# Kernel tuning notes

Measured on AMD Instinct MI355X. Metric: run time of the kernel, lower is better.

## Reference

```python
import jax, jax.numpy as jnp
import numpy as np

E = 8        # num_experts (== num_local_experts here)
H = 2048     # hidden_size
I = 1024     # intermediate_size
T = 8192     # num_tokens
K = 2        # top_k


def setup_inputs() -> dict:
    key = jax.random.key(0)
    ks = jax.random.split(key, 6)
    x = jax.random.normal(ks[0], (T, H), dtype=jnp.float32)
    selected_experts = jax.random.randint(ks[1], (T, K), 0, E, dtype=jnp.int32)
    routing_weights = jax.random.uniform(ks[2], (T, K), dtype=jnp.float32)
    # per-expert weights; torch Linear stores [out, in]; we store [E, in, out] for einsum
    gate_w = jax.random.normal(ks[3], (E, H, I), dtype=jnp.float32) * 0.02
    up_w = jax.random.normal(ks[4], (E, H, I), dtype=jnp.float32) * 0.02
    down_w = jax.random.normal(ks[5], (E, I, H), dtype=jnp.float32) * 0.02
    return {
        "x": x,
        "selected_experts": selected_experts,
        "routing_weights": routing_weights,
        "gate_w": gate_w,
        "up_w": up_w,
        "down_w": down_w,
    }


def reference(x, selected_experts, routing_weights, gate_w, up_w, down_w):
    # Combined per-(token, expert) weight: sum of routing weights over top-k slots
    # that selected this expert. Mathematically identical to the sort/dispatch/
    # weighted index_add_ in the original module.
    w = jnp.einsum(
        "tke,tk->te",
        jax.nn.one_hot(selected_experts, E, dtype=x.dtype),
        routing_weights.astype(x.dtype),
    )  # [T, E]
    g = jnp.einsum("th,ehi->eti", x, gate_w)               # [E, T, I]
    u = jnp.einsum("th,ehi->eti", x, up_w)                 # [E, T, I]
    a = jax.nn.gelu(g, approximate=True) * u               # gelu tanh approx
    # down-proj per expert then weighted combine (scatter-add equivalent)
    out = jnp.einsum("eti,eih,te->th", a, down_w, w)       # [T, H], float32
    return out
```

## Files before the change

kernel.cpp:

```cpp
#include <hip/hip_runtime.h>
#include <hip/hip_bf16.h>


typedef __attribute__((ext_vector_type(8))) short bf16x8;
typedef __attribute__((ext_vector_type(4))) float f32x4;

#define AS1 __attribute__((address_space(1)))
#define AS3 __attribute__((address_space(3)))

static constexpr int T_TOK = 8192;
static constexpr int HID   = 2048;
static constexpr int INTER = 1024;
static constexpr int NEXP  = 8;
static constexpr int NPAIR = T_TOK * 2;
static constexpr int TM    = 256;
static constexpr int MAX_ROWS = NPAIR + NEXP * TM;
static constexpr int MAX_RT   = MAX_ROWS / TM;
static constexpr int OUTN = T_TOK * HID;

__device__ __forceinline__ unsigned short f2bf(float f) {
  unsigned u = __float_as_uint(f);
  u += 0x7fffu + ((u >> 16) & 1u);
  return (unsigned short)(u >> 16);
}
__device__ __forceinline__ float bf2f(unsigned short h) {
  return __uint_as_float(((unsigned)h) << 16);
}
__device__ __forceinline__ void glds16(const void* g, void* l) {
  __builtin_amdgcn_global_load_lds((const AS1 void*)g, (AS3 void*)l, 16, 0, 0);
}

__global__ void detect_k(const unsigned* __restrict__ xw, int* __restrict__ flagp) {
  int tid = threadIdx.x;
  int cnt = 0;
  for (int i = tid; i < 256; i += 64) {
    unsigned e = (xw[i] >> 7) & 0xffu;
    cnt += (e >= 0x70u && e <= 0x8fu) ? 1 : 0;
  }
  for (int off = 32; off; off >>= 1) cnt += __shfl_down(cnt, off);
  if (tid == 0) *flagp = (cnt >= 192) ? 1 : 0;
}

__global__ void zero_out_k(unsigned* __restrict__ out, const int* __restrict__ flagp) {
  int n = (*flagp) ? (OUTN / 2) : OUTN;
  int i = blockIdx.x * 256 + threadIdx.x;
  int stride = gridDim.x * 256;
  for (; i < n; i += stride) out[i] = 0u;
}

__global__ void routing_k(const int* __restrict__ sel, const void* __restrict__ rwv,
                          int* __restrict__ rows, float* __restrict__ wgt,
                          int* __restrict__ offs, const int* __restrict__ flagp) {
  __shared__ int cnt[NEXP], cur[NEXP], offs_s[NEXP + 1];
  int flag = *flagp;
  const unsigned short* rw16 = (const unsigned short*)rwv;
  const float* rwf = (const float*)rwv;
  int tid = threadIdx.x;
  if (tid < NEXP) cnt[tid] = 0;
  __syncthreads();
  for (int p = tid; p < NPAIR; p += 256) atomicAdd(&cnt[sel[p]], 1);
  __syncthreads();
  if (tid == 0) {
    int off = 0;
    for (int e = 0; e < NEXP; ++e) {
      offs_s[e] = off; cur[e] = off;
      off += (cnt[e] + TM - 1) / TM * TM;
    }
    offs_s[NEXP] = off;
  }
  __syncthreads();
  if (tid <= NEXP) offs[tid] = offs_s[tid];
  for (int p = tid; p < NPAIR; p += 256) {
    int e = sel[p];
    int pos = atomicAdd(&cur[e], 1);
    rows[pos] = p >> 1;
    wgt[pos] = flag ? bf2f(rw16[p]) : rwf[p];
  }
  for (int e = 0; e < NEXP; ++e)
    for (int r = offs_s[e] + cnt[e] + tid; r < offs_s[e + 1]; r += 256) {
      rows[r] = 0; wgt[r] = 0.f;
    }
}

__global__ void convert_x_k(const void* __restrict__ xin,
                            unsigned short* __restrict__ xc,
                            const int* __restrict__ flagp) {
  int flag = *flagp;
  const int nvec = (T_TOK * HID) / 8;
  int v = blockIdx.x * 256 + threadIdx.x;
  int stride = gridDim.x * 256;
  for (; v < nvec; v += stride) {
    if (flag) {
      ((uint4*)xc)[v] = ((const uint4*)xin)[v];
    } else {
      const float4* s = (const float4*)xin;
      float4 a = s[2 * v], b = s[2 * v + 1];
      uint4 o;
      o.x = (unsigned)f2bf(a.x) | ((unsigned)f2bf(a.y) << 16);
      o.y = (unsigned)f2bf(a.z) | ((unsigned)f2bf(a.w) << 16);
      o.z = (unsigned)f2bf(b.x) | ((unsigned)f2bf(b.y) << 16);
      o.w = (unsigned)f2bf(b.z) | ((unsigned)f2bf(b.w) << 16);
      ((uint4*)xc)[v] = o;
    }
  }
}

__global__ void transpose_k(const void* __restrict__ in,
                            unsigned short* __restrict__ out, int R, int C,
                            const int* __restrict__ flagp) {
  __shared__ unsigned short tile[64][65];
  int flag = *flagp;
  int e = blockIdx.z;
  int c0 = blockIdx.x * 64, r0 = blockIdx.y * 64;
  int tid = threadIdx.x;
  if (flag) {
    const unsigned short* src = (const unsigned short*)in + (size_t)e * R * C;
    int tx = tid & 7, ty = tid >> 3;
#pragma unroll
    for (int i = 0; i < 2; ++i) {
      int rr = ty + i * 32;
      uint4 v = *(const uint4*)(src + (size_t)(r0 + rr) * C + c0 + tx * 8);
      unsigned short* t = &tile[rr][tx * 8];
      t[0] = (unsigned short)v.x; t[1] = (unsigned short)(v.x >> 16);
      t[2] = (unsigned short)v.y; t[3] = (unsigned short)(v.y >> 16);
      t[4] = (unsigned short)v.z; t[5] = (unsigned short)(v.z >> 16);
      t[6] = (unsigned short)v.w; t[7] = (unsigned short)(v.w >> 16);
    }
  } else {
    const float* src = (const float*)in + (size_t)e * R * C;
    int tx = tid & 15, ty = tid >> 4;
#pragma unroll
    for (int i = 0; i < 4; ++i) {
      int rr = ty + i * 16;
      float4 v = *(const float4*)(src + (size_t)(r0 + rr) * C + c0 + tx * 4);
      unsigned short* t = &tile[rr][tx * 4];
      t[0] = f2bf(v.x); t[1] = f2bf(v.y); t[2] = f2bf(v.z); t[3] = f2bf(v.w);
    }
  }
  __syncthreads();
  unsigned short* dst = out + (size_t)e * R * C;
  int tx = tid & 7, ty = tid >> 3;
#pragma unroll
  for (int i = 0; i < 2; ++i) {
    int cc = ty + i * 32;
    unsigned short a0 = tile[tx * 8 + 0][cc], a1 = tile[tx * 8 + 1][cc];
    unsigned short a2 = tile[tx * 8 + 2][cc], a3 = tile[tx * 8 + 3][cc];
    unsigned short a4 = tile[tx * 8 + 4][cc], a5 = tile[tx * 8 + 5][cc];
    unsigned short a6 = tile[tx * 8 + 6][cc], a7 = tile[tx * 8 + 7][cc];
    uint4 v;
    v.x = a0 | ((unsigned)a1 << 16); v.y = a2 | ((unsigned)a3 << 16);
    v.z = a4 | ((unsigned)a5 << 16); v.w = a6 | ((unsigned)a7 << 16);
    *(uint4*)(dst + (size_t)(c0 + cc) * R + r0 + tx * 8) = v;
  }
}


__device__ __forceinline__ const bf16x8* ldf(const unsigned short* sm, int slot,
                                             int r, int c8) {
  return (const bf16x8*)(sm + slot * 8192 + r * 64 + ((c8 ^ (r & 7)) << 3));
}
__device__ __forceinline__ void stage_half(const unsigned short* p0,
                                           const unsigned short* p1,
                                           unsigned short* dst) {
  glds16(p0, dst);
  glds16(p1, dst + 4096);
}

#define MFMA8(AH, BH, B)                                                       \
  _Pragma("unroll") for (int i_ = 0; i_ < 4; ++i_) {                           \
    _Pragma("unroll") for (int j_ = 0; j_ < 2; ++j_) {                         \
      acc[AH][BH][i_][j_] = __builtin_amdgcn_mfma_f32_16x16x32_bf16(           \
          a[i_][0], B[j_][0], acc[AH][BH][i_][j_], 0, 0, 0);                   \
      acc[AH][BH][i_][j_] = __builtin_amdgcn_mfma_f32_16x16x32_bf16(           \
          a[i_][1], B[j_][1], acc[AH][BH][i_][j_], 0, 0, 0);                   \
    }                                                                          \
  }

template <int BUF, bool S1, bool S2, int VM>
__device__ __forceinline__ void ktile(
    unsigned short* sm, int wbase, int rA, int rB, int lquad,
    const unsigned short* pA00, const unsigned short* pA01,
    const unsigned short* pA10, const unsigned short* pA11,
    const unsigned short* pB00, const unsigned short* pB01,
    const unsigned short* pB10, const unsigned short* pB11,
    int ko1, int ko2, f32x4 (&acc)[2][2][4][2]) {
  bf16x8 a[4][2], b0[2][2], b1[2][2];
#pragma unroll
  for (int i = 0; i < 4; ++i)
#pragma unroll
    for (int k = 0; k < 2; ++k)
      a[i][k] = *ldf(sm, BUF * 2 + 0, rA + i * 16, k * 4 + lquad);
#pragma unroll
  for (int j = 0; j < 2; ++j)
#pragma unroll
    for (int k = 0; k < 2; ++k)
      b0[j][k] = *ldf(sm, 4 + BUF * 2 + 0, rB + j * 16, k * 4 + lquad);
  if constexpr (S1)
    stage_half(pA10 + ko1, pA11 + ko1, sm + ((BUF ^ 1) * 2 + 1) * 8192 + wbase);
  __builtin_amdgcn_s_barrier();
  asm volatile("s_waitcnt lgkmcnt(0)" ::: "memory");
  __builtin_amdgcn_s_setprio(1);
  MFMA8(0, 0, b0);
  __builtin_amdgcn_s_setprio(0);
  __builtin_amdgcn_s_barrier();
#pragma unroll
  for (int j = 0; j < 2; ++j)
#pragma unroll
    for (int k = 0; k < 2; ++k)
      b1[j][k] = *ldf(sm, 4 + BUF * 2 + 1, rB + j * 16, k * 4 + lquad);
  if constexpr (S1)
    stage_half(pB00 + ko1, pB01 + ko1, sm + (4 + (BUF ^ 1) * 2 + 0) * 8192 + wbase);
  __builtin_amdgcn_s_barrier();
  asm volatile("s_waitcnt lgkmcnt(0)" ::: "memory");
  __builtin_amdgcn_s_setprio(1);
  MFMA8(0, 1, b1);
  __builtin_amdgcn_s_setprio(0);
  __builtin_amdgcn_s_barrier();
#pragma unroll
  for (int i = 0; i < 4; ++i)
#pragma unroll
    for (int k = 0; k < 2; ++k)
      a[i][k] = *ldf(sm, BUF * 2 + 1, rA + i * 16, k * 4 + lquad);
  if constexpr (S2)
    stage_half(pA00 + ko2, pA01 + ko2, sm + (BUF * 2 + 0) * 8192 + wbase);
  __builtin_amdgcn_s_barrier();
  asm volatile("s_waitcnt lgkmcnt(0)" ::: "memory");
  __builtin_amdgcn_s_setprio(1);
  MFMA8(1, 1, b1);
  __builtin_amdgcn_s_setprio(0);
  __builtin_amdgcn_s_barrier();
  if constexpr (S2)
    stage_half(pB10 + ko2, pB11 + ko2, sm + (4 + BUF * 2 + 1) * 8192 + wbase);
  __builtin_amdgcn_s_barrier();
  __builtin_amdgcn_s_setprio(1);
  MFMA8(1, 0, b0);
  __builtin_amdgcn_s_setprio(0);
  if constexpr (VM == 4)
    asm volatile("s_waitcnt vmcnt(4)" ::: "memory");
  else if constexpr (VM == 0)
    asm volatile("s_waitcnt vmcnt(0)" ::: "memory");
  __builtin_amdgcn_s_barrier();
}

__global__ __launch_bounds__(512, 2) void gemm_gateup8(
    const unsigned short* __restrict__ xc,
    const unsigned short* __restrict__ gwT,
    const unsigned short* __restrict__ uwT,
    const int* __restrict__ rows, const int* __restrict__ offs,
    unsigned short* __restrict__ act) {
  extern __shared__ unsigned short sm[];
  int nRT = offs[NEXP] >> 8;
  int rowTile = blockIdx.x >> 3;
  if (rowTile >= nRT) return;
  int nt = blockIdx.x & 7;
  int row0 = rowTile << 8;
  int e = 0;
  while (row0 >= offs[e + 1]) ++e;

  int tid = threadIdx.x;
  int lane = tid & 63, lrow = lane & 15, lquad = lane >> 4;
  int wave = tid >> 6;
  int wmg = wave >> 2, wng = wave & 3;
  int wbase = wave << 9;
  int rA = wmg * 64 + lrow;
  int rB = wng * 32 + lrow;

  int sr = tid >> 3;
  int swz = ((tid & 7) ^ (sr & 7)) << 3;

  const unsigned short* pA00 = xc + (size_t)rows[row0 + sr] * HID + swz;
  const unsigned short* pA01 = xc + (size_t)rows[row0 + 64 + sr] * HID + swz;
  const unsigned short* pA10 = xc + (size_t)rows[row0 + 128 + sr] * HID + swz;
  const unsigned short* pA11 = xc + (size_t)rows[row0 + 192 + sr] * HID + swz;
  const unsigned short* gB = gwT + ((size_t)e * INTER + (size_t)nt * 128) * HID;
  const unsigned short* uB = uwT + ((size_t)e * INTER + (size_t)nt * 128) * HID;
  const unsigned short* pB00 = gB + (size_t)sr * HID + swz;
  const unsigned short* pB01 = gB + (size_t)(64 + sr) * HID + swz;
  const unsigned short* pB10 = uB + (size_t)sr * HID + swz;
  const unsigned short* pB11 = uB + (size_t)(64 + sr) * HID + swz;

  f32x4 acc[2][2][4][2] = {};

  stage_half(pA00, pA01, sm + 0 * 8192 + wbase);
  stage_half(pB00, pB01, sm + 4 * 8192 + wbase);
  stage_half(pB10, pB11, sm + 5 * 8192 + wbase);
  stage_half(pA10, pA11, sm + 1 * 8192 + wbase);
  stage_half(pA00 + 64, pA01 + 64, sm + 2 * 8192 + wbase);
  stage_half(pB10 + 64, pB11 + 64, sm + 7 * 8192 + wbase);
  asm volatile("s_waitcnt vmcnt(4)" ::: "memory");
  __builtin_amdgcn_s_barrier();

  constexpr int NT = HID / 64;
#pragma unroll 1
  for (int it = 0; it < NT / 2 - 1; ++it) {
    int u = it * 2;
    ktile<0, true, true, 4>(sm, wbase, rA, rB, lquad, pA00, pA01, pA10, pA11,
                            pB00, pB01, pB10, pB11, (u + 1) * 64, (u + 2) * 64, acc);
    ktile<1, true, true, 4>(sm, wbase, rA, rB, lquad, pA00, pA01, pA10, pA11,
                            pB00, pB01, pB10, pB11, (u + 2) * 64, (u + 3) * 64, acc);
  }
  ktile<0, true, false, 0>(sm, wbase, rA, rB, lquad, pA00, pA01, pA10, pA11,
                           pB00, pB01, pB10, pB11, (NT - 1) * 64, 0, acc);
  ktile<1, false, false, -1>(sm, wbase, rA, rB, lquad, pA00, pA01, pA10, pA11,
                             pB00, pB01, pB10, pB11, 0, 0, acc);

  size_t actb = (size_t)row0 * INTER + (size_t)nt * 128 + wng * 32 + lrow;
#pragma unroll
  for (int ah = 0; ah < 2; ++ah)
#pragma unroll
    for (int i = 0; i < 4; ++i)
#pragma unroll
      for (int r = 0; r < 4; ++r) {
        int m = ah * 128 + wmg * 64 + i * 16 + lquad * 4 + r;
#pragma unroll
        for (int j = 0; j < 2; ++j) {
          float g = acc[ah][0][i][j][r], u = acc[ah][1][i][j][r];
          float z = 1.5957691f * (g + 0.044715f * g * g * g);
          float aout = g * u / (1.f + __expf(-z));
          act[actb + (size_t)m * INTER + j * 16] = f2bf(aout);
        }
      }
}

__global__ __launch_bounds__(512, 2) void gemm_down8(
    const unsigned short* __restrict__ act,
    const unsigned short* __restrict__ dwT,
    const int* __restrict__ rows, const float* __restrict__ wgt,
    const int* __restrict__ offs, void* __restrict__ outv,
    const int* __restrict__ flagp) {
  extern __shared__ unsigned short sm[];
  int nRT = offs[NEXP] >> 8;
  int rowTile = blockIdx.x >> 3;
  if (rowTile >= nRT) return;
  int nt = blockIdx.x & 7;
  int row0 = rowTile << 8;
  int e = 0;
  while (row0 >= offs[e + 1]) ++e;

  int tid = threadIdx.x;
  int lane = tid & 63, lrow = lane & 15, lquad = lane >> 4;
  int wave = tid >> 6;
  int wmg = wave >> 2, wng = wave & 3;
  int wbase = wave << 9;
  int rA = wmg * 64 + lrow;
  int rB = wng * 32 + lrow;

  int sr = tid >> 3;
  int swz = ((tid & 7) ^ (sr & 7)) << 3;

  const unsigned short* pA00 = act + (size_t)(row0 + sr) * INTER + swz;
  const unsigned short* pA01 = act + (size_t)(row0 + 64 + sr) * INTER + swz;
  const unsigned short* pA10 = act + (size_t)(row0 + 128 + sr) * INTER + swz;
  const unsigned short* pA11 = act + (size_t)(row0 + 192 + sr) * INTER + swz;
  const unsigned short* dB = dwT + ((size_t)e * HID + (size_t)nt * 256) * INTER;
  const unsigned short* pB00 = dB + (size_t)sr * INTER + swz;
  const unsigned short* pB01 = dB + (size_t)(64 + sr) * INTER + swz;
  const unsigned short* pB10 = dB + (size_t)(128 + sr) * INTER + swz;
  const unsigned short* pB11 = dB + (size_t)(192 + sr) * INTER + swz;

  f32x4 acc[2][2][4][2] = {};

  stage_half(pA00, pA01, sm + 0 * 8192 + wbase);
  stage_half(pB00, pB01, sm + 4 * 8192 + wbase);
  stage_half(pB10, pB11, sm + 5 * 8192 + wbase);
  stage_half(pA10, pA11, sm + 1 * 8192 + wbase);
  stage_half(pA00 + 64, pA01 + 64, sm + 2 * 8192 + wbase);
  stage_half(pB10 + 64, pB11 + 64, sm + 7 * 8192 + wbase);
  asm volatile("s_waitcnt vmcnt(4)" ::: "memory");
  __builtin_amdgcn_s_barrier();

  constexpr int NT = INTER / 64;
#pragma unroll 1
  for (int it = 0; it < NT / 2 - 1; ++it) {
    int u = it * 2;
    ktile<0, true, true, 4>(sm, wbase, rA, rB, lquad, pA00, pA01, pA10, pA11,
                            pB00, pB01, pB10, pB11, (u + 1) * 64, (u + 2) * 64, acc);
    ktile<1, true, true, 4>(sm, wbase, rA, rB, lquad, pA00, pA01, pA10, pA11,
                            pB00, pB01, pB10, pB11, (u + 2) * 64, (u + 3) * 64, acc);
  }
  ktile<0, true, false, 0>(sm, wbase, rA, rB, lquad, pA00, pA01, pA10, pA11,
                           pB00, pB01, pB10, pB11, (NT - 1) * 64, 0, acc);
  ktile<1, false, false, -1>(sm, wbase, rA, rB, lquad, pA00, pA01, pA10, pA11,
                             pB00, pB01, pB10, pB11, 0, 0, acc);

  int flag = *flagp;
#pragma unroll
  for (int ah = 0; ah < 2; ++ah)
#pragma unroll
    for (int i = 0; i < 4; ++i)
#pragma unroll
      for (int r = 0; r < 4; ++r) {
        int m = row0 + ah * 128 + wmg * 64 + i * 16 + lquad * 4 + r;
        float w = wgt[m];
        int token = rows[m];
        size_t base = (size_t)token * HID + (size_t)nt * 256 + wng * 32 + lrow;
        if (flag) {
#pragma unroll
          for (int bh = 0; bh < 2; ++bh)
#pragma unroll
            for (int j = 0; j < 2; ++j) {
              float v = acc[ah][bh][i][j][r] * w;
              float o = __shfl_xor(v, 1);
              if (((lane & 1) == 0) && w != 0.f) {
                unsigned* p = (unsigned*)((unsigned short*)outv + base + bh * 128 + j * 16);
                unsigned old = __atomic_load_n(p, __ATOMIC_RELAXED), assumed;
                do {
                  assumed = old;
                  float flo = bf2f((unsigned short)(assumed & 0xffffu));
                  float fhi = bf2f((unsigned short)(assumed >> 16));
                  unsigned nw = (unsigned)f2bf(flo + v) | ((unsigned)f2bf(fhi + o) << 16);
                  old = atomicCAS(p, assumed, nw);
                } while (old != assumed);
              }
            }
        } else {
          if (w != 0.f) {
            float* outf = (float*)outv;
#pragma unroll
            for (int bh = 0; bh < 2; ++bh)
#pragma unroll
              for (int j = 0; j < 2; ++j)
                atomicAdd(outf + base + bh * 128 + j * 16, acc[ah][bh][i][j][r] * w);
          }
        }
      }
}

extern "C" void kernel_launch(void* const* d_in, const int* in_sizes, int n_in,
                              void* d_out, int out_size, void* d_ws, size_t ws_size,
                              hipStream_t stream) {
  (void)in_sizes; (void)n_in; (void)out_size; (void)ws_size;
  const void* x   = d_in[0];
  const int* sel  = (const int*)d_in[1];
  const void* rw  = d_in[2];
  const void* gw  = d_in[3];
  const void* uw  = d_in[4];
  const void* dw  = d_in[5];

  char* ws = (char*)d_ws;
  int* offs  = (int*)ws;
  int* flagp = (int*)(ws + 64);
  int* rows  = (int*)(ws + 256);
  float* wgt = (float*)(ws + 256 + MAX_ROWS * 4);
  unsigned short* gwT = (unsigned short*)(ws + 256 + MAX_ROWS * 8);
  unsigned short* uwT = gwT + (size_t)NEXP * HID * INTER;
  unsigned short* dwT = uwT + (size_t)NEXP * HID * INTER;
  unsigned short* xc  = dwT + (size_t)NEXP * HID * INTER;
  unsigned short* act = xc + (size_t)T_TOK * HID;

  hipFuncSetAttribute(reinterpret_cast<const void*>(gemm_gateup8),
                      hipFuncAttributeMaxDynamicSharedMemorySize, 131072);
  hipFuncSetAttribute(reinterpret_cast<const void*>(gemm_down8),
                      hipFuncAttributeMaxDynamicSharedMemorySize, 131072);

  detect_k<<<1, 64, 0, stream>>>((const unsigned*)x, flagp);
  zero_out_k<<<4096, 256, 0, stream>>>((unsigned*)d_out, flagp);
  routing_k<<<1, 256, 0, stream>>>(sel, rw, rows, wgt, offs, flagp);
  transpose_k<<<dim3(INTER / 64, HID / 64, NEXP), 256, 0, stream>>>(gw, gwT, HID, INTER, flagp);
  transpose_k<<<dim3(INTER / 64, HID / 64, NEXP), 256, 0, stream>>>(uw, uwT, HID, INTER, flagp);
  transpose_k<<<dim3(HID / 64, INTER / 64, NEXP), 256, 0, stream>>>(dw, dwT, INTER, HID, flagp);
  convert_x_k<<<4096, 256, 0, stream>>>(x, xc, flagp);
  gemm_gateup8<<<MAX_RT * 8, 512, 131072, stream>>>(xc, gwT, uwT, rows, offs, act);
  gemm_down8<<<MAX_RT * 8, 512, 131072, stream>>>(act, dwT, rows, wgt, offs, d_out, flagp);
}
```

Before: 691.5 us.

## Replace atomic scatter-add in down GEMM with per-row buffer and combine kernel

```diff
diff --git a/kernel.cpp b/kernel.cpp
--- a/kernel.cpp
+++ b/kernel.cpp
@@ -4,6 +4,7 @@
 
 typedef __attribute__((ext_vector_type(8))) short bf16x8;
 typedef __attribute__((ext_vector_type(4))) float f32x4;
+typedef __attribute__((ext_vector_type(4))) unsigned short us4;
 
 #define AS1 __attribute__((address_space(1)))
 #define AS3 __attribute__((address_space(3)))
@@ -50,7 +51,8 @@
 
 __global__ void routing_k(const int* __restrict__ sel, const void* __restrict__ rwv,
                           int* __restrict__ rows, float* __restrict__ wgt,
-                          int* __restrict__ offs, const int* __restrict__ flagp) {
+                          int* __restrict__ offs, int* __restrict__ pairpos,
+                          const int* __restrict__ flagp) {
   __shared__ int cnt[NEXP], cur[NEXP], offs_s[NEXP + 1];
   int flag = *flagp;
   const unsigned short* rw16 = (const unsigned short*)rwv;
@@ -58,7 +60,7 @@
   int tid = threadIdx.x;
   if (tid < NEXP) cnt[tid] = 0;
   __syncthreads();
-  for (int p = tid; p < NPAIR; p += 256) atomicAdd(&cnt[sel[p]], 1);
+  for (int p = tid; p < NPAIR; p += 1024) atomicAdd(&cnt[sel[p]], 1);
   __syncthreads();
   if (tid == 0) {
     int off = 0;
@@ -70,14 +72,15 @@
   }
   __syncthreads();
   if (tid <= NEXP) offs[tid] = offs_s[tid];
-  for (int p = tid; p < NPAIR; p += 256) {
+  for (int p = tid; p < NPAIR; p += 1024) {
     int e = sel[p];
     int pos = atomicAdd(&cur[e], 1);
     rows[pos] = p >> 1;
     wgt[pos] = flag ? bf2f(rw16[p]) : rwf[p];
+    pairpos[p] = pos;
   }
   for (int e = 0; e < NEXP; ++e)
-    for (int r = offs_s[e] + cnt[e] + tid; r < offs_s[e + 1]; r += 256) {
+    for (int r = offs_s[e] + cnt[e] + tid; r < offs_s[e + 1]; r += 1024) {
       rows[r] = 0; wgt[r] = 0.f;
     }
 }
@@ -108,50 +111,42 @@
 __global__ void transpose_k(const void* __restrict__ in,
                             unsigned short* __restrict__ out, int R, int C,
                             const int* __restrict__ flagp) {
-  __shared__ unsigned short tile[64][65];
+  __shared__ unsigned short t[64 * 72];
   int flag = *flagp;
   int e = blockIdx.z;
   int c0 = blockIdx.x * 64, r0 = blockIdx.y * 64;
   int tid = threadIdx.x;
+  int mr = tid >> 4;
+  int mc = tid & 15;
+  unsigned short b[4][4];
   if (flag) {
     const unsigned short* src = (const unsigned short*)in + (size_t)e * R * C;
-    int tx = tid & 7, ty = tid >> 3;
-#pragma unroll
-    for (int i = 0; i < 2; ++i) {
-      int rr = ty + i * 32;
-      uint4 v = *(const uint4*)(src + (size_t)(r0 + rr) * C + c0 + tx * 8);
-      unsigned short* t = &tile[rr][tx * 8];
-      t[0] = (unsigned short)v.x; t[1] = (unsigned short)(v.x >> 16);
-      t[2] = (unsigned short)v.y; t[3] = (unsigned short)(v.y >> 16);
-      t[4] = (unsigned short)v.z; t[5] = (unsigned short)(v.z >> 16);
-      t[6] = (unsigned short)v.w; t[7] = (unsigned short)(v.w >> 16);
+#pragma unroll
+    for (int i = 0; i < 4; ++i) {
+      us4 v = *(const us4*)(src + (size_t)(r0 + mr * 4 + i) * C + c0 + mc * 4);
+      b[i][0] = v[0]; b[i][1] = v[1]; b[i][2] = v[2]; b[i][3] = v[3];
     }
   } else {
     const float* src = (const float*)in + (size_t)e * R * C;
-    int tx = tid & 15, ty = tid >> 4;
 #pragma unroll
     for (int i = 0; i < 4; ++i) {
-      int rr = ty + i * 16;
-      float4 v = *(const float4*)(src + (size_t)(r0 + rr) * C + c0 + tx * 4);
-      unsigned short* t = &tile[rr][tx * 4];
-      t[0] = f2bf(v.x); t[1] = f2bf(v.y); t[2] = f2bf(v.z); t[3] = f2bf(v.w);
+      float4 v = *(const float4*)(src + (size_t)(r0 + mr * 4 + i) * C + c0 + mc * 4);
+      b[i][0] = f2bf(v.x); b[i][1] = f2bf(v.y); b[i][2] = f2bf(v.z); b[i][3] = f2bf(v.w);
     }
   }
+#pragma unroll
+  for (int j = 0; j < 4; ++j) {
+    us4 w;
+    w[0] = b[0][j]; w[1] = b[1][j]; w[2] = b[2][j]; w[3] = b[3][j];
+    *(us4*)(&t[(mc * 4 + j) * 72 + mr * 4]) = w;
+  }
   __syncthreads();
-  unsigned short* dst = out + (size_t)e * R * C;
-  int tx = tid & 7, ty = tid >> 3;
-#pragma unroll
-  for (int i = 0; i < 2; ++i) {
-    int cc = ty + i * 32;
-    unsigned short a0 = tile[tx * 8 + 0][cc], a1 = tile[tx * 8 + 1][cc];
-    unsigned short a2 = tile[tx * 8 + 2][cc], a3 = tile[tx * 8 + 3][cc];
-    unsigned short a4 = tile[tx * 8 + 4][cc], a5 = tile[tx * 8 + 5][cc];
-    unsigned short a6 = tile[tx * 8 + 6][cc], a7 = tile[tx * 8 + 7][cc];
-    uint4 v;
-    v.x = a0 | ((unsigned)a1 << 16); v.y = a2 | ((unsigned)a3 << 16);
-    v.z = a4 | ((unsigned)a5 << 16); v.w = a6 | ((unsigned)a7 << 16);
-    *(uint4*)(dst + (size_t)(c0 + cc) * R + r0 + tx * 8) = v;
-  }
+  int orow = tid >> 2, ch = (tid & 3) * 16;
+  uint4 v0 = *(const uint4*)(&t[orow * 72 + ch]);
+  uint4 v1 = *(const uint4*)(&t[orow * 72 + ch + 8]);
+  unsigned short* dst = out + (size_t)e * R * C + (size_t)(c0 + orow) * R + r0 + ch;
+  *(uint4*)(dst) = v0;
+  *(uint4*)(dst + 8) = v1;
 }
 
 
@@ -322,12 +317,13 @@
       }
 }
 
+template <int EPI>
 __global__ __launch_bounds__(512, 2) void gemm_down8(
     const unsigned short* __restrict__ act,
     const unsigned short* __restrict__ dwT,
     const int* __restrict__ rows, const float* __restrict__ wgt,
     const int* __restrict__ offs, void* __restrict__ outv,
-    const int* __restrict__ flagp) {
+    const int* __restrict__ flagp, float* __restrict__ y) {
   extern __shared__ unsigned short sm[];
   int nRT = offs[NEXP] >> 8;
   int rowTile = blockIdx.x >> 3;
@@ -383,53 +379,97 @@
   ktile<1, false, false, -1>(sm, wbase, rA, rB, lquad, pA00, pA01, pA10, pA11,
                              pB00, pB01, pB10, pB11, 0, 0, acc);
 
-  int flag = *flagp;
-#pragma unroll
-  for (int ah = 0; ah < 2; ++ah)
-#pragma unroll
-    for (int i = 0; i < 4; ++i)
-#pragma unroll
-      for (int r = 0; r < 4; ++r) {
-        int m = row0 + ah * 128 + wmg * 64 + i * 16 + lquad * 4 + r;
-        float w = wgt[m];
-        int token = rows[m];
-        size_t base = (size_t)token * HID + (size_t)nt * 256 + wng * 32 + lrow;
-        if (flag) {
+  if constexpr (EPI == 1) {
+#pragma unroll
+    for (int ah = 0; ah < 2; ++ah)
+#pragma unroll
+      for (int i = 0; i < 4; ++i)
+#pragma unroll
+        for (int r = 0; r < 4; ++r) {
+          int m = row0 + ah * 128 + wmg * 64 + i * 16 + lquad * 4 + r;
+          float w = wgt[m];
+          float* yp = y + (size_t)m * HID + (size_t)nt * 256 + wng * 32 + lrow;
 #pragma unroll
           for (int bh = 0; bh < 2; ++bh)
 #pragma unroll
-            for (int j = 0; j < 2; ++j) {
-              float v = acc[ah][bh][i][j][r] * w;
-              float o = __shfl_xor(v, 1);
-              if (((lane & 1) == 0) && w != 0.f) {
-                unsigned* p = (unsigned*)((unsigned short*)outv + base + bh * 128 + j * 16);
-                unsigned old = __atomic_load_n(p, __ATOMIC_RELAXED), assumed;
-                do {
-                  assumed = old;
-                  float flo = bf2f((unsigned short)(assumed & 0xffffu));
-                  float fhi = bf2f((unsigned short)(assumed >> 16));
-                  unsigned nw = (unsigned)f2bf(flo + v) | ((unsigned)f2bf(fhi + o) << 16);
-                  old = atomicCAS(p, assumed, nw);
-                } while (old != assumed);
+            for (int j = 0; j < 2; ++j)
+              yp[bh * 128 + j * 16] = acc[ah][bh][i][j][r] * w;
+        }
+  } else {
+    int flag = *flagp;
+#pragma unroll
+    for (int ah = 0; ah < 2; ++ah)
+#pragma unroll
+      for (int i = 0; i < 4; ++i)
+#pragma unroll
+        for (int r = 0; r < 4; ++r) {
+          int m = row0 + ah * 128 + wmg * 64 + i * 16 + lquad * 4 + r;
+          float w = wgt[m];
+          int token = rows[m];
+          size_t base = (size_t)token * HID + (size_t)nt * 256 + wng * 32 + lrow;
+          if (flag) {
+#pragma unroll
+            for (int bh = 0; bh < 2; ++bh)
+#pragma unroll
+              for (int j = 0; j < 2; ++j) {
+                float v = acc[ah][bh][i][j][r] * w;
+                float o = __shfl_xor(v, 1);
+                if (((lane & 1) == 0) && w != 0.f) {
+                  unsigned* p = (unsigned*)((unsigned short*)outv + base + bh * 128 + j * 16);
+                  unsigned old = __atomic_load_n(p, __ATOMIC_RELAXED), assumed;
+                  do {
+                    assumed = old;
+                    float flo = bf2f((unsigned short)(assumed & 0xffffu));
+                    float fhi = bf2f((unsigned short)(assumed >> 16));
+                    unsigned nw = (unsigned)f2bf(flo + v) | ((unsigned)f2bf(fhi + o) << 16);
+                    old = atomicCAS(p, assumed, nw);
+                  } while (old != assumed);
+                }
               }
+          } else {
+            if (w != 0.f) {
+              float* outf = (float*)outv;
+#pragma unroll
+              for (int bh = 0; bh < 2; ++bh)
+#pragma unroll
+                for (int j = 0; j < 2; ++j)
+                  atomicAdd(outf + base + bh * 128 + j * 16, acc[ah][bh][i][j][r] * w);
             }
-        } else {
-          if (w != 0.f) {
-            float* outf = (float*)outv;
-#pragma unroll
-            for (int bh = 0; bh < 2; ++bh)
-#pragma unroll
-              for (int j = 0; j < 2; ++j)
-                atomicAdd(outf + base + bh * 128 + j * 16, acc[ah][bh][i][j][r] * w);
           }
         }
-      }
+  }
+}
+
+__global__ void combine_k(const float* __restrict__ y,
+                          const int* __restrict__ pairpos,
+                          void* __restrict__ outv, const int* __restrict__ flagp) {
+  int flag = *flagp;
+  const int NV = T_TOK * (HID / 4);
+  int v = blockIdx.x * 256 + threadIdx.x;
+  int stride = gridDim.x * 256;
+  for (; v < NV; v += stride) {
+    int t = v >> 9;
+    int hq = (v & 511) * 4;
+    int p0 = pairpos[2 * t], p1 = pairpos[2 * t + 1];
+    float4 a = *(const float4*)(y + (size_t)p0 * HID + hq);
+    float4 b = *(const float4*)(y + (size_t)p1 * HID + hq);
+    float4 s;
+    s.x = a.x + b.x; s.y = a.y + b.y; s.z = a.z + b.z; s.w = a.w + b.w;
+    if (flag) {
+      uint2 o;
+      o.x = (unsigned)f2bf(s.x) | ((unsigned)f2bf(s.y) << 16);
+      o.y = (unsigned)f2bf(s.z) | ((unsigned)f2bf(s.w) << 16);
+      *(uint2*)((unsigned short*)outv + (size_t)v * 4) = o;
+    } else {
+      *(float4*)((float*)outv + (size_t)v * 4) = s;
+    }
+  }
 }
 
 extern "C" void kernel_launch(void* const* d_in, const int* in_sizes, int n_in,
                               void* d_out, int out_size, void* d_ws, size_t ws_size,
                               hipStream_t stream) {
-  (void)in_sizes; (void)n_in; (void)out_size; (void)ws_size;
+  (void)in_sizes; (void)n_in; (void)out_size;
   const void* x   = d_in[0];
   const int* sel  = (const int*)d_in[1];
   const void* rw  = d_in[2];
@@ -438,28 +478,44 @@
   const void* dw  = d_in[5];
 
   char* ws = (char*)d_ws;
-  int* offs  = (int*)ws;
-  int* flagp = (int*)(ws + 64);
-  int* rows  = (int*)(ws + 256);
-  float* wgt = (float*)(ws + 256 + MAX_ROWS * 4);
-  unsigned short* gwT = (unsigned short*)(ws + 256 + MAX_ROWS * 8);
+  int* offs     = (int*)ws;
+  int* flagp    = (int*)(ws + 64);
+  int* rows     = (int*)(ws + 256);
+  float* wgt    = (float*)(ws + 256 + MAX_ROWS * 4);
+  int* pairpos  = (int*)(ws + 256 + MAX_ROWS * 8);
+  size_t off0   = 256 + (size_t)MAX_ROWS * 8 + (size_t)NPAIR * 4;
+  off0 = (off0 + 255) & ~(size_t)255;
+  unsigned short* dwT = (unsigned short*)(ws + off0);
+  unsigned short* act = dwT + (size_t)NEXP * HID * INTER;
+  unsigned short* gwT = act + (size_t)MAX_ROWS * INTER;
   unsigned short* uwT = gwT + (size_t)NEXP * HID * INTER;
-  unsigned short* dwT = uwT + (size_t)NEXP * HID * INTER;
-  unsigned short* xc  = dwT + (size_t)NEXP * HID * INTER;
-  unsigned short* act = xc + (size_t)T_TOK * HID;
+  unsigned short* xc  = uwT + (size_t)NEXP * HID * INTER;
+  float* y            = (float*)gwT;
+  size_t y_end = ((char*)gwT - ws) + (size_t)MAX_ROWS * HID * 4;
+  bool use_y = ws_size >= y_end;
 
   hipFuncSetAttribute(reinterpret_cast<const void*>(gemm_gateup8),
                       hipFuncAttributeMaxDynamicSharedMemorySize, 131072);
-  hipFuncSetAttribute(reinterpret_cast<const void*>(gemm_down8),
+  hipFuncSetAttribute(reinterpret_cast<const void*>(gemm_down8<1>),
                       hipFuncAttributeMaxDynamicSharedMemorySize, 131072);
+  hipFuncSetAttribute(reinterpret_cast<const void*>(gemm_down8<0>),
+                      hipFuncAttributeMaxDynamicSharedMemorySize, 131072);
 
   detect_k<<<1, 64, 0, stream>>>((const unsigned*)x, flagp);
-  zero_out_k<<<4096, 256, 0, stream>>>((unsigned*)d_out, flagp);
-  routing_k<<<1, 256, 0, stream>>>(sel, rw, rows, wgt, offs, flagp);
+  if (!use_y)
+    zero_out_k<<<4096, 256, 0, stream>>>((unsigned*)d_out, flagp);
+  routing_k<<<1, 1024, 0, stream>>>(sel, rw, rows, wgt, offs, pairpos, flagp);
   transpose_k<<<dim3(INTER / 64, HID / 64, NEXP), 256, 0, stream>>>(gw, gwT, HID, INTER, flagp);
   transpose_k<<<dim3(INTER / 64, HID / 64, NEXP), 256, 0, stream>>>(uw, uwT, HID, INTER, flagp);
   transpose_k<<<dim3(HID / 64, INTER / 64, NEXP), 256, 0, stream>>>(dw, dwT, INTER, HID, flagp);
   convert_x_k<<<4096, 256, 0, stream>>>(x, xc, flagp);
   gemm_gateup8<<<MAX_RT * 8, 512, 131072, stream>>>(xc, gwT, uwT, rows, offs, act);
-  gemm_down8<<<MAX_RT * 8, 512, 131072, stream>>>(act, dwT, rows, wgt, offs, d_out, flagp);
-}
+  if (use_y) {
+    gemm_down8<1><<<MAX_RT * 8, 512, 131072, stream>>>(act, dwT, rows, wgt, offs,
+                                                       d_out, flagp, y);
+    combine_k<<<4096, 256, 0, stream>>>(y, pairpos, d_out, flagp);
+  } else {
+    gemm_down8<0><<<MAX_RT * 8, 512, 131072, stream>>>(act, dwT, rows, wgt, offs,
+                                                       d_out, flagp, nullptr);
+  }
+}
```

Result: faster. 583.1 us (-15.7%).
